# Kernel optimization log

Measured on AMD Instinct MI355X. Metric: run time of the kernel, lower is better.

Reference implementation:

```python
import jax, jax.numpy as jnp
import numpy as np

B, S, H, D = 2, 2048, 16, 128

def setup_inputs() -> dict:
    key = jax.random.key(0)
    kq, kk, kv = jax.random.split(key, 3)
    q = jax.random.normal(kq, (B, S, H, D), dtype=jnp.float32)
    k = jax.random.normal(kk, (B, S, H, D), dtype=jnp.float32)
    v = jax.random.normal(kv, (B, S, H, D), dtype=jnp.float32)
    return {"q": q, "k": k, "v": v}

def reference(q, k, v):
    # Flash-attention semantics: layout [B, S, H, D], causal mask,
    # softmax_scale = 1/sqrt(head_dim), no dropout/window/alibi/bias.
    scale = 1.0 / jnp.sqrt(jnp.asarray(q.shape[-1], dtype=q.dtype))
    # scores: [B, H, Sq, Sk]
    scores = jnp.einsum("bqhd,bkhd->bhqk", q, k) * scale
    sq, sk = q.shape[1], k.shape[1]
    causal_mask = jnp.arange(sk)[None, :] <= jnp.arange(sq)[:, None]  # [Sq, Sk]
    scores = jnp.where(causal_mask[None, None, :, :], scores, jnp.finfo(scores.dtype).min)
    probs = jax.nn.softmax(scores, axis=-1)
    out = jnp.einsum("bhqk,bkhd->bqhd", probs, v)
    return out
```

## Files before the change

kernel.cpp:

```cpp
#include <hip/hip_runtime.h>
#include <hip/hip_bf16.h>

namespace {

constexpr int Bn = 2, Sn = 2048, Hn = 16, Dn = 128;
constexpr int QBLK = 128;
constexpr int KVBLK = 32;
constexpr int RS = Hn * Dn;
constexpr float QSCALE = 0.08838834764831845f * 1.4426950408889634f;

constexpr size_t IMG_BYTES = (size_t)Bn * Hn * 64 * 8192;
constexpr size_t WS_NEED   = 2 * IMG_BYTES;

typedef __bf16 bf16x8 __attribute__((ext_vector_type(8)));
typedef __bf16 bf16x4 __attribute__((ext_vector_type(4)));
typedef float  f32x16 __attribute__((ext_vector_type(16)));

__device__ __forceinline__ f32x16 mfma32(bf16x8 a, bf16x8 b, f32x16 c) {
  return __builtin_amdgcn_mfma_f32_32x32x16_bf16(a, b, c, 0, 0, 0);
}
__device__ __forceinline__ unsigned pack2(float a, float b) {
  union { __bf16 h[2]; unsigned u; } r;
  r.h[0] = (__bf16)a; r.h[1] = (__bf16)b;
  return r.u;
}
__device__ __forceinline__ float pair_max(float x, int hi) {
  auto r = __builtin_amdgcn_permlane32_swap(__float_as_uint(x), __float_as_uint(x), false, false);
  const float sw = __uint_as_float(hi ? r[0] : r[1]);
  return fmaxf(x, sw);
}
__device__ __forceinline__ float pair_sum(float x, int hi) {
  auto r = __builtin_amdgcn_permlane32_swap(__float_as_uint(x), __float_as_uint(x), false, false);
  const float sw = __uint_as_float(hi ? r[0] : r[1]);
  return x + sw;
}
__device__ __forceinline__ float f4e(const float4& v, int j) {
  return j == 0 ? v.x : j == 1 ? v.y : j == 2 ? v.z : v.w;
}
__device__ __forceinline__ float lane_bcast(int row, float v) {
  return __uint_as_float(__builtin_amdgcn_ds_bpermute(row * 4, __float_as_uint(v)));
}

__device__ __forceinline__ void cp16(const char* g, char* l) {
  __builtin_amdgcn_global_load_lds(
      (const __attribute__((address_space(1))) void*)g,
      (__attribute__((address_space(3))) void*)l, 16, 0, 0);
}

__device__ __forceinline__ void dma_barrier() {
  __builtin_amdgcn_sched_barrier(0);
  asm volatile("s_waitcnt vmcnt(0) lgkmcnt(0)" ::: "memory");
  __builtin_amdgcn_s_barrier();
  __builtin_amdgcn_sched_barrier(0);
}
__device__ __forceinline__ void pipeline_barrier() {
  __builtin_amdgcn_sched_barrier(0);
  asm volatile("s_waitcnt lgkmcnt(0)" ::: "memory");
  __builtin_amdgcn_s_barrier();
  __builtin_amdgcn_sched_barrier(0);
}

__global__ __launch_bounds__(256)
void prep_kv(const float* __restrict__ K, const float* __restrict__ V,
             __bf16* __restrict__ KI, __bf16* __restrict__ VI)
{
  const int gid  = (int)blockIdx.x * 256 + (int)threadIdx.x;
  const int half = gid >> 20;
  const int id   = gid & ((1 << 20) - 1);
  const int chunk = id >> 9;
  const int rem   = id & 511;
  const int bh = chunk >> 6, c = chunk & 63;
  const int b = bh >> 4, h = bh & 15;
  if (half == 0) {
    const int key = rem >> 4, dblk = rem & 15;
    const float* src = K + ((size_t)b * Sn + (size_t)c * 32 + key) * RS + h * Dn + dblk * 8;
    float4 a  = *(const float4*)src;
    float4 c2 = *(const float4*)(src + 4);
    bf16x8 f;
    f[0] = (__bf16)a.x;  f[1] = (__bf16)a.y;  f[2] = (__bf16)a.z;  f[3] = (__bf16)a.w;
    f[4] = (__bf16)c2.x; f[5] = (__bf16)c2.y; f[6] = (__bf16)c2.z; f[7] = (__bf16)c2.w;
    char* dst = (char*)KI + (size_t)chunk * 8192 + ((key * 256 + dblk * 16) ^ ((key & 7) << 4));
    *(bf16x8*)dst = f;
  } else {
    const int d = rem >> 2, koct = rem & 3;
    const float* src = V + ((size_t)b * Sn + (size_t)c * 32 + koct * 8) * RS + h * Dn + d;
    bf16x8 f;
#pragma unroll
    for (int j = 0; j < 8; ++j) f[j] = (__bf16)src[(size_t)j * RS];
    const int off = (d * 64 + koct * 16) ^ ((d & 3) << 4) ^ (((d >> 3) & 1) << 6);
    *(bf16x8*)((char*)VI + (size_t)chunk * 8192 + off) = f;
  }
}

__global__ __launch_bounds__(512)
void fa_fwd_dma(const float* __restrict__ Q, const __bf16* __restrict__ KI,
                const __bf16* __restrict__ VI, float* __restrict__ O)
{
  __shared__ __align__(16) __bf16 Klds[8][4096];
  __shared__ __align__(16) __bf16 Vt[8][4096];

  const int tid  = threadIdx.x;
  const int lane = tid & 63;
  const int wave = tid >> 6;
  const int col  = lane & 31;
  const int hi   = lane >> 5;
  const int grp  = wave >> 2;
  const int wq   = wave & 3;

  const int xcd  = (int)blockIdx.x & 7;
  const int s    = (int)blockIdx.x >> 3;
  const int hidx = xcd * 4 + (s & 3);
  const int b    = hidx >> 4, h = hidx & 15;
  const int p    = s >> 2;
  const size_t base = ((size_t)b * Sn) * RS + (size_t)h * Dn;

  const char* KIc = (const char*)KI + (size_t)hidx * 64 * 8192;
  const char* VIc = (const char*)VI + (size_t)hidx * 64 * 8192;

  auto stageKc = [&](int cc) {
    const char* g = KIc + (size_t)cc * 8192 + lane * 16;
    char* l = (char*)&Klds[cc & 7][0];
#pragma unroll
    for (int i = 0; i < 8; ++i) cp16(g + i * 1024, l + i * 1024);
  };
  auto stageVc = [&](int cc) {
    const char* g = VIc + (size_t)cc * 8192 + lane * 16;
    char* l = (char*)&Vt[cc & 7][0];
#pragma unroll
    for (int i = 0; i < 8; ++i) cp16(g + i * 1024, l + i * 1024);
  };

  const int cswz = (col & 7) << 4;
  const int vswz = ((col & 3) << 4) ^ (((col >> 3) & 1) << 6);

#define QK8(kbp, acc) { \
  __builtin_amdgcn_s_setprio(1); \
  _Pragma("unroll") \
  for (int kk = 0; kk < 8; ++kk) { \
    bf16x8 ka = *(const bf16x8*)((kbp) + ((col * 256 + kk * 32 + hi * 16) ^ cswz)); \
    acc = mfma32(ka, qf[kk], acc); \
  } \
  __builtin_amdgcn_s_setprio(0); }

#pragma unroll 1
  for (int tp = 0; tp < 2; ++tp) {
    const int qt  = tp ? p : (15 - p);
    const int q0w = qt * QBLK + wq * 32;
    const int T   = qt + 1;

    bf16x8 qf[8];
    {
      const float* qp = Q + base + (size_t)(q0w + col) * RS + hi * 8;
#pragma unroll
      for (int kk = 0; kk < 8; ++kk) {
        float4 a = *(const float4*)(qp + kk * 16);
        float4 c2 = *(const float4*)(qp + kk * 16 + 4);
        bf16x8 f;
        f[0] = (__bf16)(a.x * QSCALE);  f[1] = (__bf16)(a.y * QSCALE);
        f[2] = (__bf16)(a.z * QSCALE);  f[3] = (__bf16)(a.w * QSCALE);
        f[4] = (__bf16)(c2.x * QSCALE); f[5] = (__bf16)(c2.y * QSCALE);
        f[6] = (__bf16)(c2.z * QSCALE); f[7] = (__bf16)(c2.w * QSCALE);
        qf[kk] = f;
      }
    }

    f32x16 o0 = {}, o1 = {}, o2 = {}, o3 = {};
    float m = -1e30f, l = 0.f;

    if (wave < 4) stageKc(wave); else stageVc(wave - 4);
    if (T > 1 && wave < 4) stageKc(4 + wave);
    dma_barrier();

    f32x16 sc0 = {}, sc1 = {};
    {
      const int cc = 2 * grp;
      if (cc * 32 <= q0w + 31) {
        const char* kb = (const char*)&Klds[cc][0];
        QK8(kb, sc0)
        if ((cc + 1) * 32 <= q0w + 31) {
          const char* kb1 = (const char*)&Klds[cc + 1][0];
          QK8(kb1, sc1)
        }
      }
    }
    dma_barrier();

#pragma unroll 1
    for (int t = 0; t < T; ++t) {
      if (t + 2 < T && wave < 4) stageKc(4 * (t + 2) + wave);
      if (t + 1 < T && wave >= 4) stageVc(4 * (t + 1) + (wave - 4));

      f32x16 sn0 = {}, sn1 = {};
      if (t + 1 < T) {
        const int cc = 4 * (t + 1) + 2 * grp;
        if (cc * 32 <= q0w + 31) {
          const char* kb = (const char*)&Klds[cc & 7][0];
          QK8(kb, sn0)
          if ((cc + 1) * 32 <= q0w + 31) {
            const char* kb1 = (const char*)&Klds[(cc + 1) & 7][0];
            QK8(kb1, sn1)
          }
        }
      }

      const int cc0 = 4 * t + 2 * grp;
      const int kv0 = cc0 * 32;
      if (kv0 <= q0w + 31) {
        const bool v1 = (kv0 + 32) <= q0w + 31;

        if (kv0 + 31 > q0w) {
          const int qk = q0w + col - kv0;
#pragma unroll
          for (int r = 0; r < 16; ++r) {
            const int krow = (r & 3) + 8 * (r >> 2) + 4 * hi;
            sc0[r] = (krow <= qk) ? sc0[r] : -1e30f;
          }
        }
        if (v1 && kv0 + 63 > q0w) {
          const int qk1 = q0w + col - (kv0 + 32);
#pragma unroll
          for (int r = 0; r < 16; ++r) {
            const int krow = (r & 3) + 8 * (r >> 2) + 4 * hi;
            sc1[r] = (krow <= qk1) ? sc1[r] : -1e30f;
          }
        }

        float t8[8];
#pragma unroll
        for (int r = 0; r < 8; ++r) t8[r] = fmaxf(sc0[r], sc0[r + 8]);
        if (v1) {
#pragma unroll
          for (int r = 0; r < 8; ++r) t8[r] = fmaxf(t8[r], fmaxf(sc1[r], sc1[r + 8]));
        }
#pragma unroll
        for (int r = 0; r < 4; ++r) t8[r] = fmaxf(t8[r], t8[r + 4]);
        const float pmax = pair_max(fmaxf(fmaxf(t8[0], t8[1]), fmaxf(t8[2], t8[3])), hi);

        if (!__all(pmax <= m + 11.0f)) {
          const float mnew = fmaxf(m, pmax);
          const float al = __builtin_amdgcn_exp2f(m - mnew);
          m = mnew;
          l *= al;
#pragma unroll
          for (int r = 0; r < 16; ++r) {
            const int row = (r & 3) + 8 * (r >> 2) + 4 * hi;
            const float ar = lane_bcast(row, al);
            o0[r] *= ar; o1[r] *= ar; o2[r] *= ar; o3[r] *= ar;
          }
        }

        float s4[4] = {0.f, 0.f, 0.f, 0.f};
#pragma unroll
        for (int r = 0; r < 16; ++r) {
          sc0[r] = __builtin_amdgcn_exp2f(sc0[r] - m);
          s4[r & 3] += sc0[r];
        }
        if (v1) {
#pragma unroll
          for (int r = 0; r < 16; ++r) {
            sc1[r] = __builtin_amdgcn_exp2f(sc1[r] - m);
            s4[r & 3] += sc1[r];
          }
        }
        l += pair_sum((s4[0] + s4[1]) + (s4[2] + s4[3]), hi);

        union { unsigned u[4]; bf16x8 v; } pa0, pa1, pb0, pb1;
        {
          unsigned cw[8];
#pragma unroll
          for (int i = 0; i < 8; ++i) cw[i] = pack2(sc0[2 * i], sc0[2 * i + 1]);
          auto s02 = __builtin_amdgcn_permlane32_swap(cw[0], cw[2], false, false);
          auto s13 = __builtin_amdgcn_permlane32_swap(cw[1], cw[3], false, false);
          auto s46 = __builtin_amdgcn_permlane32_swap(cw[4], cw[6], false, false);
          auto s57 = __builtin_amdgcn_permlane32_swap(cw[5], cw[7], false, false);
          pa0.u[0] = s02[0]; pa0.u[2] = s02[1];
          pa0.u[1] = s13[0]; pa0.u[3] = s13[1];
          pa1.u[0] = s46[0]; pa1.u[2] = s46[1];
          pa1.u[1] = s57[0]; pa1.u[3] = s57[1];
        }
        if (v1) {
          unsigned cw[8];
#pragma unroll
          for (int i = 0; i < 8; ++i) cw[i] = pack2(sc1[2 * i], sc1[2 * i + 1]);
          auto s02 = __builtin_amdgcn_permlane32_swap(cw[0], cw[2], false, false);
          auto s13 = __builtin_amdgcn_permlane32_swap(cw[1], cw[3], false, false);
          auto s46 = __builtin_amdgcn_permlane32_swap(cw[4], cw[6], false, false);
          auto s57 = __builtin_amdgcn_permlane32_swap(cw[5], cw[7], false, false);
          pb0.u[0] = s02[0]; pb0.u[2] = s02[1];
          pb0.u[1] = s13[0]; pb0.u[3] = s13[1];
          pb1.u[0] = s46[0]; pb1.u[2] = s46[1];
          pb1.u[1] = s57[0]; pb1.u[3] = s57[1];
        }

        const char* vb0 = (const char*)&Vt[cc0 & 7][0];
        const char* vb1 = (const char*)&Vt[(cc0 + 1) & 7][0];
        __builtin_amdgcn_s_setprio(1);
#pragma unroll
        for (int ks = 0; ks < 2; ++ks) {
          const bf16x8 pa = ks ? pa1.v : pa0.v;
#define PV_STEP(ovar, dt, vbp) { \
          bf16x8 vf = *(const bf16x8*)((vbp) + ((((dt)*32 + col) * 64 + ks * 32 + hi * 16) ^ vswz)); \
          ovar = mfma32(pa, vf, ovar); }
          PV_STEP(o0, 0, vb0) PV_STEP(o1, 1, vb0) PV_STEP(o2, 2, vb0) PV_STEP(o3, 3, vb0)
        }
        if (v1) {
#pragma unroll
          for (int ks = 0; ks < 2; ++ks) {
            const bf16x8 pa = ks ? pb1.v : pb0.v;
            PV_STEP(o0, 0, vb1) PV_STEP(o1, 1, vb1) PV_STEP(o2, 2, vb1) PV_STEP(o3, 3, vb1)
#undef PV_STEP
          }
        }
        __builtin_amdgcn_s_setprio(0);
      }
      dma_barrier();
      sc0 = sn0; sc1 = sn1;
    }

    float* ob  = reinterpret_cast<float*>(&Klds[0][0]);
    float* mlb = reinterpret_cast<float*>(&Vt[0][0]);
    if (grp == 1) {
      mlb[wq * 128 + lane] = m;
      mlb[wq * 128 + 64 + lane] = l;
#pragma unroll
      for (int r = 0; r < 16; ++r) {
        ob[wq * 1024 + r * 64 + lane] = o0[r];
        ob[4096 + wq * 1024 + r * 64 + lane] = o1[r];
      }
    }
    __syncthreads();
    float f0 = 1.f, f1 = 0.f;
    if (grp == 0) {
      const float m1 = mlb[wq * 128 + lane];
      const float l1 = mlb[wq * 128 + 64 + lane];
      const float mS = fmaxf(m, m1);
      f0 = __builtin_amdgcn_exp2f(m - mS);
      f1 = __builtin_amdgcn_exp2f(m1 - mS);
      l = l * f0 + l1 * f1;
#pragma unroll
      for (int r = 0; r < 16; ++r) {
        const int row = (r & 3) + 8 * (r >> 2) + 4 * hi;
        const float a0 = lane_bcast(row, f0), a1 = lane_bcast(row, f1);
        o0[r] = o0[r] * a0 + ob[wq * 1024 + r * 64 + lane] * a1;
        o1[r] = o1[r] * a0 + ob[4096 + wq * 1024 + r * 64 + lane] * a1;
      }
    }
    __syncthreads();
    if (grp == 1) {
#pragma unroll
      for (int r = 0; r < 16; ++r) {
        ob[wq * 1024 + r * 64 + lane] = o2[r];
        ob[4096 + wq * 1024 + r * 64 + lane] = o3[r];
      }
    }
    __syncthreads();
    if (grp == 0) {
#pragma unroll
      for (int r = 0; r < 16; ++r) {
        const int row = (r & 3) + 8 * (r >> 2) + 4 * hi;
        const float a0 = lane_bcast(row, f0), a1 = lane_bcast(row, f1);
        o2[r] = o2[r] * a0 + ob[wq * 1024 + r * 64 + lane] * a1;
        o3[r] = o3[r] * a0 + ob[4096 + wq * 1024 + r * 64 + lane] * a1;
      }
      const float linv = 1.0f / l;
#pragma unroll
      for (int r = 0; r < 16; ++r) {
        const int row = (r & 3) + 8 * (r >> 2) + 4 * hi;
        const float lr = lane_bcast(row, linv);
        float* op = O + base + (size_t)(q0w + row) * RS + col;
        op[0]  = o0[r] * lr;
        op[32] = o1[r] * lr;
        op[64] = o2[r] * lr;
        op[96] = o3[r] * lr;
      }
    }
    __syncthreads();
  }
#undef QK8
}

__global__ __launch_bounds__(512)
void fa_fwd_reg(const float* __restrict__ Q, const float* __restrict__ K,
                const float* __restrict__ V, float* __restrict__ O)
{
  __shared__ __align__(16) __bf16 Klds[6][KVBLK * 128];
  __shared__ __align__(16) __bf16 Vt[4][128 * KVBLK];

  const int tid  = threadIdx.x;
  const int lane = tid & 63;
  const int wave = tid >> 6;
  const int col  = lane & 31;
  const int hi   = lane >> 5;
  const int grp  = wave >> 2;
  const int wq   = wave & 3;

  const int xcd  = (int)blockIdx.x & 7;
  const int s    = (int)blockIdx.x >> 3;
  const int hidx = xcd * 4 + (s & 3);
  const int b    = hidx >> 4, h = hidx & 15;
  const int s2   = s >> 2;
  const int qt   = (s < 32) ? (15 - s2) : (s2 - 8);
  const int q0w  = qt * QBLK + wq * 32;
  const int T    = 2 * (qt + 1);
  const size_t base = ((size_t)b * Sn) * RS + (size_t)h * Dn;

  const int sthalf = tid >> 8, ht = tid & 255;
  const int skey = ht >> 3, sd = (ht & 7) * 16;
  const int vkey4 = (ht & 7) * 4, vd4 = (ht >> 3) * 4;

  float4 kr[4], vr[4];
  auto loadK = [&](int ss) {
    const int kv0 = (2 * ss + sthalf) * KVBLK;
    const float* kp = K + base + (size_t)(kv0 + skey) * RS + sd;
#pragma unroll
    for (int i = 0; i < 4; ++i) kr[i] = *(const float4*)(kp + 4 * i);
  };
  auto loadV = [&](int ss) {
    const int kv0 = (2 * ss + sthalf) * KVBLK;
    const float* vp = V + base + (size_t)(kv0 + vkey4) * RS + vd4;
#pragma unroll
    for (int i = 0; i < 4; ++i) vr[i] = *(const float4*)(vp + (size_t)i * RS);
  };
  auto stageK = [&](int ss) {
    char* kb = (char*)&Klds[(2 * ss + sthalf) % 6][0];
    const int kbase = skey * 256 + sd * 2;
    const int kswz  = (skey & 7) << 4;
#pragma unroll
    for (int i = 0; i < 2; ++i) {
      bf16x8 f;
      f[0] = (__bf16)kr[2*i].x;   f[1] = (__bf16)kr[2*i].y;
      f[2] = (__bf16)kr[2*i].z;   f[3] = (__bf16)kr[2*i].w;
      f[4] = (__bf16)kr[2*i+1].x; f[5] = (__bf16)kr[2*i+1].y;
      f[6] = (__bf16)kr[2*i+1].z; f[7] = (__bf16)kr[2*i+1].w;
      *(bf16x8*)(kb + ((kbase + 16 * i) ^ kswz)) = f;
    }
  };
  auto stageV = [&](int ss) {
    char* vb = (char*)&Vt[(2 * ss + sthalf) & 3][0];
    const int b6 = ((vd4 >> 3) & 1) << 6;
#pragma unroll
    for (int j = 0; j < 4; ++j) {
      bf16x4 w;
      w[0] = (__bf16)f4e(vr[0], j);
      w[1] = (__bf16)f4e(vr[1], j);
      w[2] = (__bf16)f4e(vr[2], j);
      w[3] = (__bf16)f4e(vr[3], j);
      const int addr = (((vd4 + j) * 64 + vkey4 * 2) ^ (j << 4)) ^ b6;
      *(bf16x4*)(vb + addr) = w;
    }
  };

  const int cswz = (col & 7) << 4;
  const int vswz = ((col & 3) << 4) ^ (((col >> 3) & 1) << 6);

  bf16x8 qf[8];
  {
    const float* qp = Q + base + (size_t)(q0w + col) * RS + hi * 8;
#pragma unroll
    for (int kk = 0; kk < 8; ++kk) {
      float4 a = *(const float4*)(qp + kk * 16);
      float4 c2 = *(const float4*)(qp + kk * 16 + 4);
      bf16x8 f;
      f[0] = (__bf16)(a.x * QSCALE);  f[1] = (__bf16)(a.y * QSCALE);
      f[2] = (__bf16)(a.z * QSCALE);  f[3] = (__bf16)(a.w * QSCALE);
      f[4] = (__bf16)(c2.x * QSCALE); f[5] = (__bf16)(c2.y * QSCALE);
      f[6] = (__bf16)(c2.z * QSCALE); f[7] = (__bf16)(c2.w * QSCALE);
      qf[kk] = f;
    }
  }

  f32x16 o0 = {}, o1 = {}, o2 = {}, o3 = {};
  float m = -1e30f, l = 0.f;

  loadK(0); loadV(0);
  stageK(0);
  loadK(1);
  stageV(0);
  loadV(1);
  stageK(1);
  if (2 < T) loadK(2);
  pipeline_barrier();

  f32x16 st_cur = {};
  if (grp * KVBLK <= q0w + 31) {
    const char* kb = (const char*)&Klds[grp][0];
    __builtin_amdgcn_s_setprio(1);
#pragma unroll
    for (int kk = 0; kk < 8; ++kk) {
      bf16x8 ka = *(const bf16x8*)(kb + ((col * 256 + kk * 32 + hi * 16) ^ cswz));
      st_cur = mfma32(ka, qf[kk], st_cur);
    }
    __builtin_amdgcn_s_setprio(0);
  }

#pragma unroll 1
  for (int t = 0; t < T; ++t) {
    f32x16 stn = {};
    const int icn = 2 * (t + 1) + grp;
    if (t + 1 < T && icn * KVBLK <= q0w + 31) {
      const char* kb = (const char*)&Klds[icn % 6][0];
      __builtin_amdgcn_s_setprio(1);
#pragma unroll
      for (int kk = 0; kk < 8; ++kk) {
        bf16x8 ka = *(const bf16x8*)(kb + ((col * 256 + kk * 32 + hi * 16) ^ cswz));
        stn = mfma32(ka, qf[kk], stn);
      }
      __builtin_amdgcn_s_setprio(0);
    }

    if (t + 2 < T) stageK(t + 2);
    if (t + 1 < T) stageV(t + 1);
    if (t + 3 < T) loadK(t + 3);
    if (t + 2 < T) loadV(t + 2);

    const int kv0 = (2 * t + grp) * KVBLK;
    if (kv0 <= q0w + 31) {
      if (kv0 + KVBLK - 1 > q0w) {
        const int qk = q0w + col - kv0;
#pragma unroll
        for (int r = 0; r < 16; ++r) {
          const int krow = (r & 3) + 8 * (r >> 2) + 4 * hi;
          st_cur[r] = (krow <= qk) ? st_cur[r] : -1e30f;
        }
      }

      float t8[8];
#pragma unroll
      for (int r = 0; r < 8; ++r) t8[r] = fmaxf(st_cur[r], st_cur[r + 8]);
#pragma unroll
      for (int r = 0; r < 4; ++r) t8[r] = fmaxf(t8[r], t8[r + 4]);
      const float pmax = pair_max(fmaxf(fmaxf(t8[0], t8[1]), fmaxf(t8[2], t8[3])), hi);

      if (!__all(pmax <= m + 11.0f)) {
        const float mnew = fmaxf(m, pmax);
        const float al = __builtin_amdgcn_exp2f(m - mnew);
        m = mnew;
        l *= al;
#pragma unroll
        for (int r = 0; r < 16; ++r) {
          const int row = (r & 3) + 8 * (r >> 2) + 4 * hi;
          const float ar = lane_bcast(row, al);
          o0[r] *= ar; o1[r] *= ar; o2[r] *= ar; o3[r] *= ar;
        }
      }

      float s4[4] = {0.f, 0.f, 0.f, 0.f};
#pragma unroll
      for (int r = 0; r < 16; ++r) {
        st_cur[r] = __builtin_amdgcn_exp2f(st_cur[r] - m);
        s4[r & 3] += st_cur[r];
      }
      l += pair_sum((s4[0] + s4[1]) + (s4[2] + s4[3]), hi);

      unsigned cw[8];
#pragma unroll
      for (int i = 0; i < 8; ++i) cw[i] = pack2(st_cur[2 * i], st_cur[2 * i + 1]);
      union { unsigned u[4]; bf16x8 v; } pa0, pa1;
      {
        auto s02 = __builtin_amdgcn_permlane32_swap(cw[0], cw[2], false, false);
        auto s13 = __builtin_amdgcn_permlane32_swap(cw[1], cw[3], false, false);
        auto s46 = __builtin_amdgcn_permlane32_swap(cw[4], cw[6], false, false);
        auto s57 = __builtin_amdgcn_permlane32_swap(cw[5], cw[7], false, false);
        pa0.u[0] = s02[0]; pa0.u[2] = s02[1];
        pa0.u[1] = s13[0]; pa0.u[3] = s13[1];
        pa1.u[0] = s46[0]; pa1.u[2] = s46[1];
        pa1.u[1] = s57[0]; pa1.u[3] = s57[1];
      }

      const char* vb = (const char*)&Vt[(2 * t + grp) & 3][0];
      __builtin_amdgcn_s_setprio(1);
#pragma unroll
      for (int ks = 0; ks < 2; ++ks) {
        const bf16x8 pa = ks ? pa1.v : pa0.v;
#define PV_STEP(ovar, dt) { \
        bf16x8 vf = *(const bf16x8*)(vb + ((((dt)*32 + col) * 64 + ks * 32 + hi * 16) ^ vswz)); \
        ovar = mfma32(pa, vf, ovar); }
        PV_STEP(o0, 0) PV_STEP(o1, 1) PV_STEP(o2, 2) PV_STEP(o3, 3)
#undef PV_STEP
      }
      __builtin_amdgcn_s_setprio(0);
    }
    pipeline_barrier();
    st_cur = stn;
  }

  float* ob  = reinterpret_cast<float*>(&Klds[0][0]);
  float* mlb = reinterpret_cast<float*>(&Vt[0][0]);
  if (grp == 1) {
    mlb[wq * 128 + lane] = m;
    mlb[wq * 128 + 64 + lane] = l;
#pragma unroll
    for (int r = 0; r < 16; ++r) {
      ob[wq * 1024 + r * 64 + lane] = o0[r];
      ob[4096 + wq * 1024 + r * 64 + lane] = o1[r];
    }
  }
  __syncthreads();
  float f0 = 1.f, f1 = 0.f;
  if (grp == 0) {
    const float m1 = mlb[wq * 128 + lane];
    const float l1 = mlb[wq * 128 + 64 + lane];
    const float mS = fmaxf(m, m1);
    f0 = __builtin_amdgcn_exp2f(m - mS);
    f1 = __builtin_amdgcn_exp2f(m1 - mS);
    l = l * f0 + l1 * f1;
#pragma unroll
    for (int r = 0; r < 16; ++r) {
      const int row = (r & 3) + 8 * (r >> 2) + 4 * hi;
      const float a0 = lane_bcast(row, f0), a1 = lane_bcast(row, f1);
      o0[r] = o0[r] * a0 + ob[wq * 1024 + r * 64 + lane] * a1;
      o1[r] = o1[r] * a0 + ob[4096 + wq * 1024 + r * 64 + lane] * a1;
    }
  }
  __syncthreads();
  if (grp == 1) {
#pragma unroll
    for (int r = 0; r < 16; ++r) {
      ob[wq * 1024 + r * 64 + lane] = o2[r];
      ob[4096 + wq * 1024 + r * 64 + lane] = o3[r];
    }
  }
  __syncthreads();
  if (grp == 0) {
#pragma unroll
    for (int r = 0; r < 16; ++r) {
      const int row = (r & 3) + 8 * (r >> 2) + 4 * hi;
      const float a0 = lane_bcast(row, f0), a1 = lane_bcast(row, f1);
      o2[r] = o2[r] * a0 + ob[wq * 1024 + r * 64 + lane] * a1;
      o3[r] = o3[r] * a0 + ob[4096 + wq * 1024 + r * 64 + lane] * a1;
    }
    const float linv = 1.0f / l;
#pragma unroll
    for (int r = 0; r < 16; ++r) {
      const int row = (r & 3) + 8 * (r >> 2) + 4 * hi;
      const float lr = lane_bcast(row, linv);
      float* op = O + base + (size_t)(q0w + row) * RS + col;
      op[0]  = o0[r] * lr;
      op[32] = o1[r] * lr;
      op[64] = o2[r] * lr;
      op[96] = o3[r] * lr;
    }
  }
}

}

extern "C" void kernel_launch(void* const* d_in, const int* , int ,
                              void* d_out, int , void* d_ws, size_t ws_size,
                              hipStream_t stream) {
  const float* q = (const float*)d_in[0];
  const float* k = (const float*)d_in[1];
  const float* v = (const float*)d_in[2];
  float* o = (float*)d_out;
  if (d_ws != nullptr && ws_size >= WS_NEED) {
    __bf16* ki = (__bf16*)d_ws;
    __bf16* vi = (__bf16*)((char*)d_ws + IMG_BYTES);
    hipLaunchKernelGGL(prep_kv, dim3(8192), dim3(256), 0, stream, k, v, ki, vi);
    hipLaunchKernelGGL(fa_fwd_dma, dim3(256), dim3(512), 0, stream, q, ki, vi, o);
  } else {
    hipLaunchKernelGGL(fa_fwd_reg, dim3(512), dim3(512), 0, stream, q, k, v, o);
  }
}
```

Before: 97.30 us.

## Split causal KV range across two blocks and merge partials in a separate kernel

Adds a split-KV path. fa_split runs 512 blocks instead of 256, and each block processes half of the KV range for a pair of query tiles. It writes unnormalized partial outputs plus running max and sum to workspace, and a new fa_merge kernel combines them. The aim is to fill more CUs and balance the causal work more evenly. The cost is an extra kernel launch and a round-trip of partial results through global memory. The fallback path is reworked into a four-group pairwise reduction kernel, which only runs when the workspace is too small, and the register-staging kernel is removed.

```diff
diff --git a/kernel.cpp b/kernel.cpp
--- a/kernel.cpp
+++ b/kernel.cpp
@@ -12,8 +12,11 @@
 constexpr size_t IMG_BYTES = (size_t)Bn * Hn * 64 * 8192;
 constexpr size_t WS_NEED   = 2 * IMG_BYTES;
 
+constexpr size_t PART_SLOT_F   = 16896;
+constexpr size_t PART_TILE_F   = 2 * PART_SLOT_F;
+constexpr size_t SPLIT_WS_NEED = 2 * IMG_BYTES + (size_t)512 * PART_TILE_F * 4;
+
 typedef __bf16 bf16x8 __attribute__((ext_vector_type(8)));
-typedef __bf16 bf16x4 __attribute__((ext_vector_type(4)));
 typedef float  f32x16 __attribute__((ext_vector_type(16)));
 
 __device__ __forceinline__ f32x16 mfma32(bf16x8 a, bf16x8 b, f32x16 c) {
@@ -34,9 +37,6 @@
   const float sw = __uint_as_float(hi ? r[0] : r[1]);
   return x + sw;
 }
-__device__ __forceinline__ float f4e(const float4& v, int j) {
-  return j == 0 ? v.x : j == 1 ? v.y : j == 2 ? v.z : v.w;
-}
 __device__ __forceinline__ float lane_bcast(int row, float v) {
   return __uint_as_float(__builtin_amdgcn_ds_bpermute(row * 4, __float_as_uint(v)));
 }
@@ -50,12 +50,6 @@
 __device__ __forceinline__ void dma_barrier() {
   __builtin_amdgcn_sched_barrier(0);
   asm volatile("s_waitcnt vmcnt(0) lgkmcnt(0)" ::: "memory");
-  __builtin_amdgcn_s_barrier();
-  __builtin_amdgcn_sched_barrier(0);
-}
-__device__ __forceinline__ void pipeline_barrier() {
-  __builtin_amdgcn_sched_barrier(0);
-  asm volatile("s_waitcnt lgkmcnt(0)" ::: "memory");
   __builtin_amdgcn_s_barrier();
   __builtin_amdgcn_sched_barrier(0);
 }
@@ -93,8 +87,299 @@
 }
 
 __global__ __launch_bounds__(512)
-void fa_fwd_dma(const float* __restrict__ Q, const __bf16* __restrict__ KI,
-                const __bf16* __restrict__ VI, float* __restrict__ O)
+void fa_split(const float* __restrict__ Q, const __bf16* __restrict__ KI,
+              const __bf16* __restrict__ VI, float* __restrict__ WP)
+{
+  __shared__ __align__(16) __bf16 Klds[4][4096];
+  __shared__ __align__(16) __bf16 Vt[4][4096];
+
+  const int tid  = threadIdx.x;
+  const int lane = tid & 63;
+  const int wave = tid >> 6;
+  const int col  = lane & 31;
+  const int hi   = lane >> 5;
+  const int grp  = wave >> 2;
+  const int wq   = wave & 3;
+
+  const int xcd  = (int)blockIdx.x & 7;
+  const int s    = (int)blockIdx.x >> 3;
+  const int hidx = xcd * 4 + (s & 3);
+  const int b    = hidx >> 4, h = hidx & 15;
+  const int pr   = (s >> 2) & 7;
+  const int role = (s >> 2) >> 3;
+  const size_t base = ((size_t)b * Sn) * RS + (size_t)h * Dn;
+
+  const char* KIc = (const char*)KI + (size_t)hidx * 64 * 8192;
+  const char* VIc = (const char*)VI + (size_t)hidx * 64 * 8192;
+
+  const int sr = wave >> 1;
+  const int hb = (wave & 1) * 4096;
+  auto stageK2 = [&](int ss) {
+    if (sr < 2) {
+      const int ck = 2 * ss + sr;
+      const char* g = KIc + (size_t)ck * 8192 + hb;
+      char* l = (char*)&Klds[ck & 3][0] + hb;
+#pragma unroll
+      for (int i = 0; i < 4; ++i) cp16(g + i * 1024 + lane * 16, l + i * 1024);
+    }
+  };
+  auto stageV2 = [&](int ss) {
+    if (sr >= 2) {
+      const int cv = 2 * ss + (sr - 2);
+      const char* g = VIc + (size_t)cv * 8192 + hb;
+      char* l = (char*)&Vt[cv & 3][0] + hb;
+#pragma unroll
+      for (int i = 0; i < 4; ++i) cp16(g + i * 1024 + lane * 16, l + i * 1024);
+    }
+  };
+
+  const int cswz = (col & 7) << 4;
+  const int vswz = ((col & 3) << 4) ^ (((col >> 3) & 1) << 6);
+
+#pragma unroll 1
+  for (int half = 0; half < 2; ++half) {
+    const int qt    = half ? pr : (15 - pr);
+    const int Th    = half ? (pr + 1) : (16 - pr);
+    const int lower = (role == half);
+    const int t0 = lower ? 0 : Th;
+    const int t1 = t0 + Th;
+    const int q0w = qt * QBLK + wq * 32;
+
+    bf16x8 qf[8];
+    {
+      const float* qp = Q + base + (size_t)(q0w + col) * RS + hi * 8;
+#pragma unroll
+      for (int kk = 0; kk < 8; ++kk) {
+        float4 a = *(const float4*)(qp + kk * 16);
+        float4 c2 = *(const float4*)(qp + kk * 16 + 4);
+        bf16x8 f;
+        f[0] = (__bf16)(a.x * QSCALE);  f[1] = (__bf16)(a.y * QSCALE);
+        f[2] = (__bf16)(a.z * QSCALE);  f[3] = (__bf16)(a.w * QSCALE);
+        f[4] = (__bf16)(c2.x * QSCALE); f[5] = (__bf16)(c2.y * QSCALE);
+        f[6] = (__bf16)(c2.z * QSCALE); f[7] = (__bf16)(c2.w * QSCALE);
+        qf[kk] = f;
+      }
+    }
+
+    f32x16 o0 = {}, o1 = {}, o2 = {}, o3 = {};
+    float m = -1e30f, l = 0.f;
+
+    stageK2(t0);
+    stageV2(t0);
+    if (t0 + 1 < t1) stageK2(t0 + 1);
+    dma_barrier();
+
+    f32x16 st_cur = {};
+    if ((2 * t0 + grp) * KVBLK <= q0w + 31) {
+      const char* kb = (const char*)&Klds[(2 * t0 + grp) & 3][0];
+      __builtin_amdgcn_s_setprio(1);
+#pragma unroll
+      for (int kk = 0; kk < 8; ++kk) {
+        bf16x8 ka = *(const bf16x8*)(kb + ((col * 256 + kk * 32 + hi * 16) ^ cswz));
+        st_cur = mfma32(ka, qf[kk], st_cur);
+      }
+      __builtin_amdgcn_s_setprio(0);
+    }
+    dma_barrier();
+
+#pragma unroll 1
+    for (int t = t0; t < t1; ++t) {
+      if (t + 2 < t1) stageK2(t + 2);
+      if (t + 1 < t1) stageV2(t + 1);
+
+      f32x16 stn = {};
+      const int icn = 2 * (t + 1) + grp;
+      if (t + 1 < t1 && icn * KVBLK <= q0w + 31) {
+        const char* kb = (const char*)&Klds[icn & 3][0];
+        __builtin_amdgcn_s_setprio(1);
+#pragma unroll
+        for (int kk = 0; kk < 8; ++kk) {
+          bf16x8 ka = *(const bf16x8*)(kb + ((col * 256 + kk * 32 + hi * 16) ^ cswz));
+          stn = mfma32(ka, qf[kk], stn);
+        }
+        __builtin_amdgcn_s_setprio(0);
+      }
+
+      const int kv0 = (2 * t + grp) * KVBLK;
+      if (kv0 <= q0w + 31) {
+        if (kv0 + KVBLK - 1 > q0w) {
+          const int qk = q0w + col - kv0;
+#pragma unroll
+          for (int r = 0; r < 16; ++r) {
+            const int krow = (r & 3) + 8 * (r >> 2) + 4 * hi;
+            st_cur[r] = (krow <= qk) ? st_cur[r] : -1e30f;
+          }
+        }
+
+        float t8[8];
+#pragma unroll
+        for (int r = 0; r < 8; ++r) t8[r] = fmaxf(st_cur[r], st_cur[r + 8]);
+#pragma unroll
+        for (int r = 0; r < 4; ++r) t8[r] = fmaxf(t8[r], t8[r + 4]);
+        const float pmax = pair_max(fmaxf(fmaxf(t8[0], t8[1]), fmaxf(t8[2], t8[3])), hi);
+
+        if (!__all(pmax <= m + 11.0f)) {
+          const float mnew = fmaxf(m, pmax);
+          const float al = __builtin_amdgcn_exp2f(m - mnew);
+          m = mnew;
+          l *= al;
+#pragma unroll
+          for (int r = 0; r < 16; ++r) {
+            const int row = (r & 3) + 8 * (r >> 2) + 4 * hi;
+            const float ar = lane_bcast(row, al);
+            o0[r] *= ar; o1[r] *= ar; o2[r] *= ar; o3[r] *= ar;
+          }
+        }
+
+        float s4[4] = {0.f, 0.f, 0.f, 0.f};
+#pragma unroll
+        for (int r = 0; r < 16; ++r) {
+          st_cur[r] = __builtin_amdgcn_exp2f(st_cur[r] - m);
+          s4[r & 3] += st_cur[r];
+        }
+        l += pair_sum((s4[0] + s4[1]) + (s4[2] + s4[3]), hi);
+
+        unsigned cw[8];
+#pragma unroll
+        for (int i = 0; i < 8; ++i) cw[i] = pack2(st_cur[2 * i], st_cur[2 * i + 1]);
+        union { unsigned u[4]; bf16x8 v; } pa0, pa1;
+        {
+          auto s02 = __builtin_amdgcn_permlane32_swap(cw[0], cw[2], false, false);
+          auto s13 = __builtin_amdgcn_permlane32_swap(cw[1], cw[3], false, false);
+          auto s46 = __builtin_amdgcn_permlane32_swap(cw[4], cw[6], false, false);
+          auto s57 = __builtin_amdgcn_permlane32_swap(cw[5], cw[7], false, false);
+          pa0.u[0] = s02[0]; pa0.u[2] = s02[1];
+          pa0.u[1] = s13[0]; pa0.u[3] = s13[1];
+          pa1.u[0] = s46[0]; pa1.u[2] = s46[1];
+          pa1.u[1] = s57[0]; pa1.u[3] = s57[1];
+        }
+
+        const char* vb = (const char*)&Vt[(2 * t + grp) & 3][0];
+        __builtin_amdgcn_s_setprio(1);
+#pragma unroll
+        for (int ks = 0; ks < 2; ++ks) {
+          const bf16x8 pa = ks ? pa1.v : pa0.v;
+#define PV_STEP(ovar, dt) { \
+          bf16x8 vf = *(const bf16x8*)(vb + ((((dt)*32 + col) * 64 + ks * 32 + hi * 16) ^ vswz)); \
+          ovar = mfma32(pa, vf, ovar); }
+          PV_STEP(o0, 0) PV_STEP(o1, 1) PV_STEP(o2, 2) PV_STEP(o3, 3)
+#undef PV_STEP
+        }
+        __builtin_amdgcn_s_setprio(0);
+      }
+      dma_barrier();
+      st_cur = stn;
+    }
+
+    float* ob  = reinterpret_cast<float*>(&Klds[0][0]);
+    float* mlb = reinterpret_cast<float*>(&Vt[0][0]);
+    if (grp == 1) {
+      mlb[wq * 128 + lane] = m;
+      mlb[wq * 128 + 64 + lane] = l;
+#pragma unroll
+      for (int r = 0; r < 16; ++r) {
+        ob[wq * 1024 + r * 64 + lane] = o0[r];
+        ob[4096 + wq * 1024 + r * 64 + lane] = o1[r];
+      }
+    }
+    __syncthreads();
+    float f0 = 1.f, f1 = 0.f;
+    if (grp == 0) {
+      const float m1 = mlb[wq * 128 + lane];
+      const float l1 = mlb[wq * 128 + 64 + lane];
+      const float mS = fmaxf(m, m1);
+      f0 = __builtin_amdgcn_exp2f(m - mS);
+      f1 = __builtin_amdgcn_exp2f(m1 - mS);
+      m = mS;
+      l = l * f0 + l1 * f1;
+#pragma unroll
+      for (int r = 0; r < 16; ++r) {
+        const int row = (r & 3) + 8 * (r >> 2) + 4 * hi;
+        const float a0 = lane_bcast(row, f0), a1 = lane_bcast(row, f1);
+        o0[r] = o0[r] * a0 + ob[wq * 1024 + r * 64 + lane] * a1;
+        o1[r] = o1[r] * a0 + ob[4096 + wq * 1024 + r * 64 + lane] * a1;
+      }
+    }
+    __syncthreads();
+    if (grp == 1) {
+#pragma unroll
+      for (int r = 0; r < 16; ++r) {
+        ob[wq * 1024 + r * 64 + lane] = o2[r];
+        ob[4096 + wq * 1024 + r * 64 + lane] = o3[r];
+      }
+    }
+    __syncthreads();
+
+    const int tix = hidx * 16 + qt;
+    float* W = WP + (size_t)tix * PART_TILE_F + (lower ? 0 : PART_SLOT_F);
+    if (grp == 0) {
+#pragma unroll
+      for (int r = 0; r < 16; ++r) {
+        const int row = (r & 3) + 8 * (r >> 2) + 4 * hi;
+        const float a0 = lane_bcast(row, f0), a1 = lane_bcast(row, f1);
+        o2[r] = o2[r] * a0 + ob[wq * 1024 + r * 64 + lane] * a1;
+        o3[r] = o3[r] * a0 + ob[4096 + wq * 1024 + r * 64 + lane] * a1;
+        float* wp = W + (size_t)(wq * 32 + row) * 128 + col;
+        wp[0]  = o0[r];
+        wp[32] = o1[r];
+        wp[64] = o2[r];
+        wp[96] = o3[r];
+      }
+      if (hi == 0) {
+        W[16384 + wq * 32 + col] = m;
+        W[16512 + wq * 32 + col] = l;
+      }
+    }
+    __syncthreads();
+  }
+}
+
+__global__ __launch_bounds__(256)
+void fa_merge(const float* __restrict__ WP, float* __restrict__ O)
+{
+  const int tix  = (int)blockIdx.x;
+  const int hidx = tix >> 4, qt = tix & 15;
+  const int b = hidx >> 4, h = hidx & 15;
+  const size_t base = ((size_t)b * Sn) * RS + (size_t)h * Dn;
+  const int q0 = qt * QBLK;
+  const float* W0 = WP + (size_t)tix * PART_TILE_F;
+  const float* W1 = W0 + PART_SLOT_F;
+
+  __shared__ float a0s[128], a1s[128];
+  const int t = threadIdx.x;
+  if (t < 128) {
+    const float m0 = W0[16384 + t], l0 = W0[16512 + t];
+    const float m1 = W1[16384 + t], l1 = W1[16512 + t];
+    const float M  = fmaxf(m0, m1);
+    const float c0 = __builtin_amdgcn_exp2f(m0 - M);
+    const float c1 = __builtin_amdgcn_exp2f(m1 - M);
+    const float li = 1.0f / (l0 * c0 + l1 * c1);
+    a0s[t] = c0 * li;
+    a1s[t] = c1 * li;
+  }
+  __syncthreads();
+
+#pragma unroll
+  for (int i = 0; i < 16; ++i) {
+    const int fl   = t + 256 * i;
+    const int elem = fl * 4;
+    const int r    = elem >> 7;
+    const int d    = elem & 127;
+    const float4 p0 = *(const float4*)(W0 + elem);
+    const float4 p1 = *(const float4*)(W1 + elem);
+    const float a0 = a0s[r], a1 = a1s[r];
+    float4 o;
+    o.x = p0.x * a0 + p1.x * a1;
+    o.y = p0.y * a0 + p1.y * a1;
+    o.z = p0.z * a0 + p1.z * a1;
+    o.w = p0.w * a0 + p1.w * a1;
+    *(float4*)(O + base + (size_t)(q0 + r) * RS + d) = o;
+  }
+}
+
+__global__ __launch_bounds__(512)
+void fa_fwd_pair(const float* __restrict__ Q, const __bf16* __restrict__ KI,
+                 const __bf16* __restrict__ VI, float* __restrict__ O)
 {
   __shared__ __align__(16) __bf16 Klds[8][4096];
   __shared__ __align__(16) __bf16 Vt[8][4096];
@@ -319,328 +604,116 @@
 
     float* ob  = reinterpret_cast<float*>(&Klds[0][0]);
     float* mlb = reinterpret_cast<float*>(&Vt[0][0]);
-    if (grp == 1) {
-      mlb[wq * 128 + lane] = m;
-      mlb[wq * 128 + 64 + lane] = l;
-#pragma unroll
-      for (int r = 0; r < 16; ++r) {
-        ob[wq * 1024 + r * 64 + lane] = o0[r];
-        ob[4096 + wq * 1024 + r * 64 + lane] = o1[r];
-      }
-    }
-    __syncthreads();
     float f0 = 1.f, f1 = 0.f;
-    if (grp == 0) {
-      const float m1 = mlb[wq * 128 + lane];
-      const float l1 = mlb[wq * 128 + 64 + lane];
-      const float mS = fmaxf(m, m1);
-      f0 = __builtin_amdgcn_exp2f(m - mS);
-      f1 = __builtin_amdgcn_exp2f(m1 - mS);
-      l = l * f0 + l1 * f1;
-#pragma unroll
-      for (int r = 0; r < 16; ++r) {
-        const int row = (r & 3) + 8 * (r >> 2) + 4 * hi;
-        const float a0 = lane_bcast(row, f0), a1 = lane_bcast(row, f1);
-        o0[r] = o0[r] * a0 + ob[wq * 1024 + r * 64 + lane] * a1;
-        o1[r] = o1[r] * a0 + ob[4096 + wq * 1024 + r * 64 + lane] * a1;
-      }
-    }
-    __syncthreads();
-    if (grp == 1) {
-#pragma unroll
-      for (int r = 0; r < 16; ++r) {
-        ob[wq * 1024 + r * 64 + lane] = o2[r];
-        ob[4096 + wq * 1024 + r * 64 + lane] = o3[r];
-      }
-    }
-    __syncthreads();
-    if (grp == 0) {
-#pragma unroll
-      for (int r = 0; r < 16; ++r) {
-        const int row = (r & 3) + 8 * (r >> 2) + 4 * hi;
-        const float a0 = lane_bcast(row, f0), a1 = lane_bcast(row, f1);
-        o2[r] = o2[r] * a0 + ob[wq * 1024 + r * 64 + lane] * a1;
-        o3[r] = o3[r] * a0 + ob[4096 + wq * 1024 + r * 64 + lane] * a1;
-      }
-      const float linv = 1.0f / l;
-#pragma unroll
-      for (int r = 0; r < 16; ++r) {
-        const int row = (r & 3) + 8 * (r >> 2) + 4 * hi;
-        const float lr = lane_bcast(row, linv);
-        float* op = O + base + (size_t)(q0w + row) * RS + col;
-        op[0]  = o0[r] * lr;
-        op[32] = o1[r] * lr;
-        op[64] = o2[r] * lr;
-        op[96] = o3[r] * lr;
+    {
+      const int src = grp & 1;
+      float* obr = ob  + (grp >> 1) * 8192;
+      float* mlr = mlb + (grp >> 1) * 512;
+      if (src) {
+        mlr[wq * 128 + lane] = m;
+        mlr[wq * 128 + 64 + lane] = l;
+#pragma unroll
+        for (int r = 0; r < 16; ++r) {
+          obr[wq * 1024 + r * 64 + lane] = o0[r];
+          obr[4096 + wq * 1024 + r * 64 + lane] = o1[r];
+        }
+      }
+      __syncthreads();
+      if (!src) {
+        const float m1 = mlr[wq * 128 + lane];
+        const float l1 = mlr[wq * 128 + 64 + lane];
+        const float mS = fmaxf(m, m1);
+        f0 = __builtin_amdgcn_exp2f(m - mS);
+        f1 = __builtin_amdgcn_exp2f(m1 - mS);
+        m = mS;
+        l = l * f0 + l1 * f1;
+#pragma unroll
+        for (int r = 0; r < 16; ++r) {
+          const int row = (r & 3) + 8 * (r >> 2) + 4 * hi;
+          const float a0 = lane_bcast(row, f0), a1 = lane_bcast(row, f1);
+          o0[r] = o0[r] * a0 + obr[wq * 1024 + r * 64 + lane] * a1;
+          o1[r] = o1[r] * a0 + obr[4096 + wq * 1024 + r * 64 + lane] * a1;
+        }
+      }
+      __syncthreads();
+      if (src) {
+#pragma unroll
+        for (int r = 0; r < 16; ++r) {
+          obr[wq * 1024 + r * 64 + lane] = o2[r];
+          obr[4096 + wq * 1024 + r * 64 + lane] = o3[r];
+        }
+      }
+      __syncthreads();
+      if (!src) {
+#pragma unroll
+        for (int r = 0; r < 16; ++r) {
+          const int row = (r & 3) + 8 * (r >> 2) + 4 * hi;
+          const float a0 = lane_bcast(row, f0), a1 = lane_bcast(row, f1);
+          o2[r] = o2[r] * a0 + obr[wq * 1024 + r * 64 + lane] * a1;
+          o3[r] = o3[r] * a0 + obr[4096 + wq * 1024 + r * 64 + lane] * a1;
+        }
+      }
+      __syncthreads();
+    }
+    {
+      if (grp == 2) {
+        mlb[wq * 128 + lane] = m;
+        mlb[wq * 128 + 64 + lane] = l;
+#pragma unroll
+        for (int r = 0; r < 16; ++r) {
+          ob[wq * 1024 + r * 64 + lane] = o0[r];
+          ob[4096 + wq * 1024 + r * 64 + lane] = o1[r];
+        }
+      }
+      __syncthreads();
+      if (grp == 0) {
+        const float m1 = mlb[wq * 128 + lane];
+        const float l1 = mlb[wq * 128 + 64 + lane];
+        const float mS = fmaxf(m, m1);
+        f0 = __builtin_amdgcn_exp2f(m - mS);
+        f1 = __builtin_amdgcn_exp2f(m1 - mS);
+        l = l * f0 + l1 * f1;
+#pragma unroll
+        for (int r = 0; r < 16; ++r) {
+          const int row = (r & 3) + 8 * (r >> 2) + 4 * hi;
+          const float a0 = lane_bcast(row, f0), a1 = lane_bcast(row, f1);
+          o0[r] = o0[r] * a0 + ob[wq * 1024 + r * 64 + lane] * a1;
+          o1[r] = o1[r] * a0 + ob[4096 + wq * 1024 + r * 64 + lane] * a1;
+        }
+      }
+      __syncthreads();
+      if (grp == 2) {
+#pragma unroll
+        for (int r = 0; r < 16; ++r) {
+          ob[wq * 1024 + r * 64 + lane] = o2[r];
+          ob[4096 + wq * 1024 + r * 64 + lane] = o3[r];
+        }
+      }
+      __syncthreads();
+      if (grp == 0) {
+#pragma unroll
+        for (int r = 0; r < 16; ++r) {
+          const int row = (r & 3) + 8 * (r >> 2) + 4 * hi;
+          const float a0 = lane_bcast(row, f0), a1 = lane_bcast(row, f1);
+          o2[r] = o2[r] * a0 + ob[wq * 1024 + r * 64 + lane] * a1;
+          o3[r] = o3[r] * a0 + ob[4096 + wq * 1024 + r * 64 + lane] * a1;
+        }
+        const float linv = 1.0f / l;
+#pragma unroll
+        for (int r = 0; r < 16; ++r) {
+          const int row = (r & 3) + 8 * (r >> 2) + 4 * hi;
+          const float lr = lane_bcast(row, linv);
+          float* op = O + base + (size_t)(q0w + row) * RS + col;
+          op[0]  = o0[r] * lr;
+          op[32] = o1[r] * lr;
+          op[64] = o2[r] * lr;
+          op[96] = o3[r] * lr;
+        }
       }
     }
     __syncthreads();
   }
 #undef QK8
-}
-
-__global__ __launch_bounds__(512)
-void fa_fwd_reg(const float* __restrict__ Q, const float* __restrict__ K,
-                const float* __restrict__ V, float* __restrict__ O)
-{
-  __shared__ __align__(16) __bf16 Klds[6][KVBLK * 128];
-  __shared__ __align__(16) __bf16 Vt[4][128 * KVBLK];
-
-  const int tid  = threadIdx.x;
-  const int lane = tid & 63;
-  const int wave = tid >> 6;
-  const int col  = lane & 31;
-  const int hi   = lane >> 5;
-  const int grp  = wave >> 2;
-  const int wq   = wave & 3;
-
-  const int xcd  = (int)blockIdx.x & 7;
-  const int s    = (int)blockIdx.x >> 3;
-  const int hidx = xcd * 4 + (s & 3);
-  const int b    = hidx >> 4, h = hidx & 15;
-  const int s2   = s >> 2;
-  const int qt   = (s < 32) ? (15 - s2) : (s2 - 8);
-  const int q0w  = qt * QBLK + wq * 32;
-  const int T    = 2 * (qt + 1);
-  const size_t base = ((size_t)b * Sn) * RS + (size_t)h * Dn;
-
-  const int sthalf = tid >> 8, ht = tid & 255;
-  const int skey = ht >> 3, sd = (ht & 7) * 16;
-  const int vkey4 = (ht & 7) * 4, vd4 = (ht >> 3) * 4;
-
-  float4 kr[4], vr[4];
-  auto loadK = [&](int ss) {
-    const int kv0 = (2 * ss + sthalf) * KVBLK;
-    const float* kp = K + base + (size_t)(kv0 + skey) * RS + sd;
-#pragma unroll
-    for (int i = 0; i < 4; ++i) kr[i] = *(const float4*)(kp + 4 * i);
-  };
-  auto loadV = [&](int ss) {
-    const int kv0 = (2 * ss + sthalf) * KVBLK;
-    const float* vp = V + base + (size_t)(kv0 + vkey4) * RS + vd4;
-#pragma unroll
-    for (int i = 0; i < 4; ++i) vr[i] = *(const float4*)(vp + (size_t)i * RS);
-  };
-  auto stageK = [&](int ss) {
-    char* kb = (char*)&Klds[(2 * ss + sthalf) % 6][0];
-    const int kbase = skey * 256 + sd * 2;
-    const int kswz  = (skey & 7) << 4;
-#pragma unroll
-    for (int i = 0; i < 2; ++i) {
-      bf16x8 f;
-      f[0] = (__bf16)kr[2*i].x;   f[1] = (__bf16)kr[2*i].y;
-      f[2] = (__bf16)kr[2*i].z;   f[3] = (__bf16)kr[2*i].w;
-      f[4] = (__bf16)kr[2*i+1].x; f[5] = (__bf16)kr[2*i+1].y;
-      f[6] = (__bf16)kr[2*i+1].z; f[7] = (__bf16)kr[2*i+1].w;
-      *(bf16x8*)(kb + ((kbase + 16 * i) ^ kswz)) = f;
-    }
-  };
-  auto stageV = [&](int ss) {
-    char* vb = (char*)&Vt[(2 * ss + sthalf) & 3][0];
-    const int b6 = ((vd4 >> 3) & 1) << 6;
-#pragma unroll
-    for (int j = 0; j < 4; ++j) {
-      bf16x4 w;
-      w[0] = (__bf16)f4e(vr[0], j);
-      w[1] = (__bf16)f4e(vr[1], j);
-      w[2] = (__bf16)f4e(vr[2], j);
-      w[3] = (__bf16)f4e(vr[3], j);
-      const int addr = (((vd4 + j) * 64 + vkey4 * 2) ^ (j << 4)) ^ b6;
-      *(bf16x4*)(vb + addr) = w;
-    }
-  };
-
-  const int cswz = (col & 7) << 4;
-  const int vswz = ((col & 3) << 4) ^ (((col >> 3) & 1) << 6);
-
-  bf16x8 qf[8];
-  {
-    const float* qp = Q + base + (size_t)(q0w + col) * RS + hi * 8;
-#pragma unroll
-    for (int kk = 0; kk < 8; ++kk) {
-      float4 a = *(const float4*)(qp + kk * 16);
-      float4 c2 = *(const float4*)(qp + kk * 16 + 4);
-      bf16x8 f;
-      f[0] = (__bf16)(a.x * QSCALE);  f[1] = (__bf16)(a.y * QSCALE);
-      f[2] = (__bf16)(a.z * QSCALE);  f[3] = (__bf16)(a.w * QSCALE);
-      f[4] = (__bf16)(c2.x * QSCALE); f[5] = (__bf16)(c2.y * QSCALE);
-      f[6] = (__bf16)(c2.z * QSCALE); f[7] = (__bf16)(c2.w * QSCALE);
-      qf[kk] = f;
-    }
-  }
-
-  f32x16 o0 = {}, o1 = {}, o2 = {}, o3 = {};
-  float m = -1e30f, l = 0.f;
-
-  loadK(0); loadV(0);
-  stageK(0);
-  loadK(1);
-  stageV(0);
-  loadV(1);
-  stageK(1);
-  if (2 < T) loadK(2);
-  pipeline_barrier();
-
-  f32x16 st_cur = {};
-  if (grp * KVBLK <= q0w + 31) {
-    const char* kb = (const char*)&Klds[grp][0];
-    __builtin_amdgcn_s_setprio(1);
-#pragma unroll
-    for (int kk = 0; kk < 8; ++kk) {
-      bf16x8 ka = *(const bf16x8*)(kb + ((col * 256 + kk * 32 + hi * 16) ^ cswz));
-      st_cur = mfma32(ka, qf[kk], st_cur);
-    }
-    __builtin_amdgcn_s_setprio(0);
-  }
-
-#pragma unroll 1
-  for (int t = 0; t < T; ++t) {
-    f32x16 stn = {};
-    const int icn = 2 * (t + 1) + grp;
-    if (t + 1 < T && icn * KVBLK <= q0w + 31) {
-      const char* kb = (const char*)&Klds[icn % 6][0];
-      __builtin_amdgcn_s_setprio(1);
-#pragma unroll
-      for (int kk = 0; kk < 8; ++kk) {
-        bf16x8 ka = *(const bf16x8*)(kb + ((col * 256 + kk * 32 + hi * 16) ^ cswz));
-        stn = mfma32(ka, qf[kk], stn);
-      }
-      __builtin_amdgcn_s_setprio(0);
-    }
-
-    if (t + 2 < T) stageK(t + 2);
-    if (t + 1 < T) stageV(t + 1);
-    if (t + 3 < T) loadK(t + 3);
-    if (t + 2 < T) loadV(t + 2);
-
-    const int kv0 = (2 * t + grp) * KVBLK;
-    if (kv0 <= q0w + 31) {
-      if (kv0 + KVBLK - 1 > q0w) {
-        const int qk = q0w + col - kv0;
-#pragma unroll
-        for (int r = 0; r < 16; ++r) {
-          const int krow = (r & 3) + 8 * (r >> 2) + 4 * hi;
-          st_cur[r] = (krow <= qk) ? st_cur[r] : -1e30f;
-        }
-      }
-
-      float t8[8];
-#pragma unroll
-      for (int r = 0; r < 8; ++r) t8[r] = fmaxf(st_cur[r], st_cur[r + 8]);
-#pragma unroll
-      for (int r = 0; r < 4; ++r) t8[r] = fmaxf(t8[r], t8[r + 4]);
-      const float pmax = pair_max(fmaxf(fmaxf(t8[0], t8[1]), fmaxf(t8[2], t8[3])), hi);
-
-      if (!__all(pmax <= m + 11.0f)) {
-        const float mnew = fmaxf(m, pmax);
-        const float al = __builtin_amdgcn_exp2f(m - mnew);
-        m = mnew;
-        l *= al;
-#pragma unroll
-        for (int r = 0; r < 16; ++r) {
-          const int row = (r & 3) + 8 * (r >> 2) + 4 * hi;
-          const float ar = lane_bcast(row, al);
-          o0[r] *= ar; o1[r] *= ar; o2[r] *= ar; o3[r] *= ar;
-        }
-      }
-
-      float s4[4] = {0.f, 0.f, 0.f, 0.f};
-#pragma unroll
-      for (int r = 0; r < 16; ++r) {
-        st_cur[r] = __builtin_amdgcn_exp2f(st_cur[r] - m);
-        s4[r & 3] += st_cur[r];
-      }
-      l += pair_sum((s4[0] + s4[1]) + (s4[2] + s4[3]), hi);
-
-      unsigned cw[8];
-#pragma unroll
-      for (int i = 0; i < 8; ++i) cw[i] = pack2(st_cur[2 * i], st_cur[2 * i + 1]);
-      union { unsigned u[4]; bf16x8 v; } pa0, pa1;
-      {
-        auto s02 = __builtin_amdgcn_permlane32_swap(cw[0], cw[2], false, false);
-        auto s13 = __builtin_amdgcn_permlane32_swap(cw[1], cw[3], false, false);
-        auto s46 = __builtin_amdgcn_permlane32_swap(cw[4], cw[6], false, false);
-        auto s57 = __builtin_amdgcn_permlane32_swap(cw[5], cw[7], false, false);
-        pa0.u[0] = s02[0]; pa0.u[2] = s02[1];
-        pa0.u[1] = s13[0]; pa0.u[3] = s13[1];
-        pa1.u[0] = s46[0]; pa1.u[2] = s46[1];
-        pa1.u[1] = s57[0]; pa1.u[3] = s57[1];
-      }
-
-      const char* vb = (const char*)&Vt[(2 * t + grp) & 3][0];
-      __builtin_amdgcn_s_setprio(1);
-#pragma unroll
-      for (int ks = 0; ks < 2; ++ks) {
-        const bf16x8 pa = ks ? pa1.v : pa0.v;
-#define PV_STEP(ovar, dt) { \
-        bf16x8 vf = *(const bf16x8*)(vb + ((((dt)*32 + col) * 64 + ks * 32 + hi * 16) ^ vswz)); \
-        ovar = mfma32(pa, vf, ovar); }
-        PV_STEP(o0, 0) PV_STEP(o1, 1) PV_STEP(o2, 2) PV_STEP(o3, 3)
-#undef PV_STEP
-      }
-      __builtin_amdgcn_s_setprio(0);
-    }
-    pipeline_barrier();
-    st_cur = stn;
-  }
-
-  float* ob  = reinterpret_cast<float*>(&Klds[0][0]);
-  float* mlb = reinterpret_cast<float*>(&Vt[0][0]);
-  if (grp == 1) {
-    mlb[wq * 128 + lane] = m;
-    mlb[wq * 128 + 64 + lane] = l;
-#pragma unroll
-    for (int r = 0; r < 16; ++r) {
-      ob[wq * 1024 + r * 64 + lane] = o0[r];
-      ob[4096 + wq * 1024 + r * 64 + lane] = o1[r];
-    }
-  }
-  __syncthreads();
-  float f0 = 1.f, f1 = 0.f;
-  if (grp == 0) {
-    const float m1 = mlb[wq * 128 + lane];
-    const float l1 = mlb[wq * 128 + 64 + lane];
-    const float mS = fmaxf(m, m1);
-    f0 = __builtin_amdgcn_exp2f(m - mS);
-    f1 = __builtin_amdgcn_exp2f(m1 - mS);
-    l = l * f0 + l1 * f1;
-#pragma unroll
-    for (int r = 0; r < 16; ++r) {
-      const int row = (r & 3) + 8 * (r >> 2) + 4 * hi;
-      const float a0 = lane_bcast(row, f0), a1 = lane_bcast(row, f1);
-      o0[r] = o0[r] * a0 + ob[wq * 1024 + r * 64 + lane] * a1;
-      o1[r] = o1[r] * a0 + ob[4096 + wq * 1024 + r * 64 + lane] * a1;
-    }
-  }
-  __syncthreads();
-  if (grp == 1) {
-#pragma unroll
-    for (int r = 0; r < 16; ++r) {
-      ob[wq * 1024 + r * 64 + lane] = o2[r];
-      ob[4096 + wq * 1024 + r * 64 + lane] = o3[r];
-    }
-  }
-  __syncthreads();
-  if (grp == 0) {
-#pragma unroll
-    for (int r = 0; r < 16; ++r) {
-      const int row = (r & 3) + 8 * (r >> 2) + 4 * hi;
-      const float a0 = lane_bcast(row, f0), a1 = lane_bcast(row, f1);
-      o2[r] = o2[r] * a0 + ob[wq * 1024 + r * 64 + lane] * a1;
-      o3[r] = o3[r] * a0 + ob[4096 + wq * 1024 + r * 64 + lane] * a1;
-    }
-    const float linv = 1.0f / l;
-#pragma unroll
-    for (int r = 0; r < 16; ++r) {
-      const int row = (r & 3) + 8 * (r >> 2) + 4 * hi;
-      const float lr = lane_bcast(row, linv);
-      float* op = O + base + (size_t)(q0w + row) * RS + col;
-      op[0]  = o0[r] * lr;
-      op[32] = o1[r] * lr;
-      op[64] = o2[r] * lr;
-      op[96] = o3[r] * lr;
-    }
-  }
 }
 
 }
@@ -652,12 +725,15 @@
   const float* k = (const float*)d_in[1];
   const float* v = (const float*)d_in[2];
   float* o = (float*)d_out;
-  if (d_ws != nullptr && ws_size >= WS_NEED) {
-    __bf16* ki = (__bf16*)d_ws;
-    __bf16* vi = (__bf16*)((char*)d_ws + IMG_BYTES);
+  __bf16* ki = (__bf16*)d_ws;
+  __bf16* vi = (__bf16*)((char*)d_ws + IMG_BYTES);
+  if (d_ws != nullptr && ws_size >= SPLIT_WS_NEED) {
+    float* wp = (float*)((char*)d_ws + 2 * IMG_BYTES);
     hipLaunchKernelGGL(prep_kv, dim3(8192), dim3(256), 0, stream, k, v, ki, vi);
-    hipLaunchKernelGGL(fa_fwd_dma, dim3(256), dim3(512), 0, stream, q, ki, vi, o);
+    hipLaunchKernelGGL(fa_split, dim3(512), dim3(512), 0, stream, q, ki, vi, wp);
+    hipLaunchKernelGGL(fa_merge, dim3(512), dim3(256), 0, stream, wp, o);
   } else {
-    hipLaunchKernelGGL(fa_fwd_reg, dim3(512), dim3(512), 0, stream, q, k, v, o);
+    hipLaunchKernelGGL(prep_kv, dim3(8192), dim3(256), 0, stream, k, v, ki, vi);
+    hipLaunchKernelGGL(fa_fwd_pair, dim3(256), dim3(512), 0, stream, q, ki, vi, o);
   }
 }
```

Result: slower. 126.7 us (+30.2%).
